# Optimization experiments

Hardware: AMD Instinct MI355X
Metric: run time of the kernel (lower is better)

Reference implementation:

```python
import jax, jax.numpy as jnp
import numpy as np

NA, NB, C = 50000, 50000, 128
E = 800000
S, IN, H, NBASES = 8, 64, 64, 8
NUM_LAYERS = 2
EPS = 1e-5


def setup_inputs() -> dict:
    key = jax.random.key(0)
    ks = jax.random.split(key, 16)
    inp = {
        'x_a': jax.random.normal(ks[0], (NA, C), jnp.float32),
        'x_b': jax.random.normal(ks[1], (NB, C), jnp.float32),
        'schema_x': jax.random.normal(ks[2], (S, IN), jnp.float32),
        'edge_ab': jax.random.randint(ks[3], (2, E), 0, NA, jnp.int32),
        'edge_ba': jax.random.randint(ks[4], (2, E), 0, NA, jnp.int32),
        'edge_aa': jax.random.randint(ks[5], (2, E), 0, NA, jnp.int32),
        'schema_edge_index': jax.random.randint(ks[6], (2, 24), 0, S, jnp.int32),
        'pre_W': jax.random.normal(ks[7], (H, IN), jnp.float32) * (1.0 / np.sqrt(IN)),
        'pre_b': jnp.zeros((H,), jnp.float32),
        'gcn_W': jax.random.normal(ks[8], (H, H), jnp.float32) * (1.0 / np.sqrt(H)),
        'gcn_b': jnp.zeros((H,), jnp.float32),
        'coeff_W': jax.random.normal(ks[9], (NBASES, 2 * H), jnp.float32) * (1.0 / np.sqrt(2 * H)),
        'coeff_b': jnp.zeros((NBASES,), jnp.float32),
        'bases': jax.random.normal(ks[10], (NUM_LAYERS, NBASES, C, C), jnp.float32) * (1.0 / np.sqrt(C)),
        'sage_bias': jnp.zeros((NUM_LAYERS, 3, C), jnp.float32),
        'ln_w': jnp.ones((NUM_LAYERS, 2, C), jnp.float32),
        'ln_b': jnp.zeros((NUM_LAYERS, 2, C), jnp.float32),
    }
    return inp


def _gcn_conv(x, ei, W, b):
    # PyG GCNConv: add self-loops, symmetric normalization, then linear.
    n = x.shape[0]
    loop = jnp.arange(n, dtype=ei.dtype)
    src = jnp.concatenate([ei[0], loop])
    dst = jnp.concatenate([ei[1], loop])
    deg = jax.ops.segment_sum(jnp.ones_like(dst, jnp.float32), dst, num_segments=n)
    dinv = jax.lax.rsqrt(jnp.maximum(deg, 1e-12))
    norm = dinv[src] * dinv[dst]  # [E+n]
    xw = x @ W.T  # [n, H]
    out = jax.ops.segment_sum(xw[src] * norm[:, None], dst, num_segments=n)
    return out + b


def _sage_conv(x_src, x_dst, ei, W, b):
    # PyG SAGEConv, aggr='mean': lin_l(mean_j x_src[j]) + lin_r(x_dst); lin_l.weight == lin_r.weight == W.
    n_dst = x_dst.shape[0]
    msg_sum = jax.ops.segment_sum(x_src[ei[0]], ei[1], num_segments=n_dst)
    cnt = jax.ops.segment_sum(jnp.ones(ei.shape[1], x_src.dtype), ei[1], num_segments=n_dst)
    mean = msg_sum / jnp.maximum(cnt, 1.0)[:, None]
    return (mean + x_dst) @ W.T + b


def _layer_norm(x, w, b):
    mu = jnp.mean(x, axis=-1, keepdims=True)
    var = jnp.mean(jnp.square(x - mu), axis=-1, keepdims=True)
    return (x - mu) * jax.lax.rsqrt(var + EPS) * w + b


def _edge_weight(sf_src, sf_dst, coeff_W, coeff_b, bases_l):
    combined = jnp.concatenate([sf_src, sf_dst], axis=0)  # [2H]
    coeffs = combined @ coeff_W.T + coeff_b  # [NBASES]
    return jnp.einsum('i,ijk->jk', coeffs, bases_l)  # [C, C]


def reference(x_a, x_b, schema_x, edge_ab, edge_ba, edge_aa, schema_edge_index,
              pre_W, pre_b, gcn_W, gcn_b, coeff_W, coeff_b, bases,
              sage_bias, ln_w, ln_b):
    # Schema GCN over the tiny table-level graph. table_to_index: a->0, b->1.
    h = schema_x @ pre_W.T + pre_b
    ori = h
    sf = jax.nn.relu(_gcn_conv(h, schema_edge_index, gcn_W, gcn_b))  # [S, H]

    for l in range(NUM_LAYERS):
        bases_l = bases[l]
        W_ab = _edge_weight(sf[0], sf[1], coeff_W, coeff_b, bases_l)
        W_ba = _edge_weight(sf[1], sf[0], coeff_W, coeff_b, bases_l)
        W_aa = _edge_weight(sf[0], sf[0], coeff_W, coeff_b, bases_l)
        # HeteroConv(aggr='sum'): sum SAGE outputs per destination node type.
        out_b = _sage_conv(x_a, x_b, edge_ab, W_ab, sage_bias[l, 0])
        out_a = (_sage_conv(x_b, x_a, edge_ba, W_ba, sage_bias[l, 1])
                 + _sage_conv(x_a, x_a, edge_aa, W_aa, sage_bias[l, 2]))
        x_a = jax.nn.relu(_layer_norm(out_a, ln_w[l, 0], ln_b[l, 0]))
        x_b = jax.nn.relu(_layer_norm(out_b, ln_w[l, 1], ln_b[l, 1]))

    return x_a, x_b, sf, ori
```

## Files before the change

### kernel.cpp

```cpp
#include <hip/hip_runtime.h>

#define NA 50000
#define NB 50000
#define NN 50000
#define CDIM 128
#define EDGES 800000
#define SS 8
#define INDIM 64
#define HDIM 64
#define NBASES 8
#define NBUCK 98
#define BSH 9

typedef __attribute__((ext_vector_type(8))) short bf16x8;
typedef __attribute__((ext_vector_type(4))) float f32x4;


__device__ __forceinline__ unsigned short f2bf(float f) {
    unsigned u = __float_as_uint(f);
    return (unsigned short)((u + 0x7FFFu + ((u >> 16) & 1u)) >> 16);
}

__global__ __launch_bounds__(512) void schema_kernel(
    const float* __restrict__ schema_x, const int* __restrict__ sei,
    const float* __restrict__ preW, const float* __restrict__ preb,
    const float* __restrict__ gcnW, const float* __restrict__ gcnb,
    const float* __restrict__ coW, const float* __restrict__ cob,
    float* __restrict__ out_sf, float* __restrict__ out_ori,
    float* __restrict__ coeffs)
{
    __shared__ float h[SS][HDIM];
    __shared__ float xw[SS][HDIM];
    __shared__ float sf[SS][HDIM];
    __shared__ float deg[SS];
    __shared__ float nrm[32];
    __shared__ int es[32], ed[32];

    int t = threadIdx.x;
    int i = t >> 6, j = t & 63;

    float acc = preb[j];
    for (int k = 0; k < INDIM; k++) acc += schema_x[i * INDIM + k] * preW[j * INDIM + k];
    h[i][j] = acc;
    out_ori[i * HDIM + j] = acc;
    if (t < SS) deg[t] = 0.0f;
    __syncthreads();

    if (t < 32) {
        int s, d;
        if (t < 24) { s = sei[t]; d = sei[24 + t]; }
        else        { s = t - 24; d = t - 24; }
        es[t] = s; ed[t] = d;
        atomicAdd(&deg[d], 1.0f);
    }
    __syncthreads();
    if (t < 32) {
        nrm[t] = rsqrtf(fmaxf(deg[es[t]], 1e-12f)) * rsqrtf(fmaxf(deg[ed[t]], 1e-12f));
    }
    float a2 = 0.0f;
    for (int k = 0; k < HDIM; k++) a2 += h[i][k] * gcnW[j * HDIM + k];
    xw[i][j] = a2;
    __syncthreads();

    float o = gcnb[j];
    for (int e = 0; e < 32; e++) {
        if (ed[e] == i) o += xw[es[e]][j] * nrm[e];
    }
    float s = fmaxf(o, 0.0f);
    sf[i][j] = s;
    out_sf[i * HDIM + j] = s;
    __syncthreads();

    if (t < 24) {
        int ty = t >> 3, ii = t & 7;
        int srow = (ty == 1) ? 1 : 0;
        int drow = (ty == 0) ? 1 : 0;
        float a = cob[ii];
        for (int k = 0; k < HDIM; k++) a += sf[srow][k] * coW[ii * (2 * HDIM) + k];
        for (int k = 0; k < HDIM; k++) a += sf[drow][k] * coW[ii * (2 * HDIM) + HDIM + k];
        coeffs[ty * 8 + ii] = a;
    }
}

__global__ __launch_bounds__(256) void build_w_kernel(
    const float* __restrict__ bases, const float* __restrict__ coeffs,
    unsigned short* __restrict__ Wbf)
{
    int idx = blockIdx.x * blockDim.x + threadIdx.x;
    int lt = idx >> 14;
    int jk = idx & 16383;
    int l = lt / 3, ty = lt % 3;
    float acc = 0.0f;
#pragma unroll
    for (int i = 0; i < NBASES; i++)
        acc += coeffs[ty * 8 + i] * bases[((size_t)(l * NBASES + i) << 14) + jk];
    Wbf[idx] = f2bf(acc);
}

__global__ __launch_bounds__(256) void tobf16_kernel(
    const float* __restrict__ in, unsigned short* __restrict__ out, int n)
{
    int i = (blockIdx.x * 256 + threadIdx.x) * 4;
    if (i >= n) return;
    float4 f = *(const float4*)(in + i);
    ushort4 o;
    o.x = f2bf(f.x); o.y = f2bf(f.y); o.z = f2bf(f.z); o.w = f2bf(f.w);
    *(ushort4*)(out + i) = o;
}

__global__ __launch_bounds__(256) void zero_rows_kernel(
    unsigned short* a0, unsigned short* b0, unsigned short* a1, unsigned short* b1)
{
    int t = threadIdx.x;
    int tab = t >> 6, w = t & 63;
    unsigned short* p = (tab == 0) ? a0 : (tab == 1) ? b0 : (tab == 2) ? a1 : b1;
    ((unsigned*)(p + (size_t)NN * CDIM))[w] = 0u;
}


__global__ __launch_bounds__(256) void bucket_count_kernel(
    const int* __restrict__ ab, const int* __restrict__ ba,
    const int* __restrict__ aa, int* __restrict__ bcnt)
{
    __shared__ int h[NBUCK];
    int t = threadIdx.x;
    int ty = blockIdx.y;
    const int* ei = (ty == 0) ? ab : (ty == 1) ? ba : aa;
    if (t < NBUCK) h[t] = 0;
    __syncthreads();
    int cb = blockIdx.x * 4096;
    int en = min(cb + 4096, EDGES);
    for (int e = cb + t; e < en; e += 256)
        atomicAdd(&h[ei[EDGES + e] >> BSH], 1);
    __syncthreads();
    if (t < NBUCK) atomicAdd(&bcnt[ty * NBUCK + t], h[t]);
}

__global__ __launch_bounds__(32) void bucket_scan_kernel(
    const int* __restrict__ bcnt, int* __restrict__ boff, int* __restrict__ bcur)
{
    int t = threadIdx.x;
    if (t < 3) {
        int run = 0;
        for (int i = 0; i < NBUCK; i++) {
            int c = bcnt[t * NBUCK + i];
            boff[t * (NBUCK + 1) + i] = run;
            bcur[t * NBUCK + i] = run;
            run += c;
        }
        boff[t * (NBUCK + 1) + NBUCK] = run;
    }
}

__global__ __launch_bounds__(256) void bucket_partition_kernel(
    const int* __restrict__ ab, const int* __restrict__ ba,
    const int* __restrict__ aa, int* __restrict__ bcur,
    unsigned* __restrict__ buf)
{
    __shared__ int h[NBUCK];
    __shared__ int basearr[NBUCK];
    __shared__ int cur[NBUCK];
    int t = threadIdx.x;
    int ty = blockIdx.y;
    const int* ei = (ty == 0) ? ab : (ty == 1) ? ba : aa;
    if (t < NBUCK) h[t] = 0;
    __syncthreads();
    int cb = blockIdx.x * 4096;
    int en = min(cb + 4096, EDGES);
    for (int e = cb + t; e < en; e += 256)
        atomicAdd(&h[ei[EDGES + e] >> BSH], 1);
    __syncthreads();
    if (t < NBUCK) {
        basearr[t] = atomicAdd(&bcur[ty * NBUCK + t], h[t]);
        cur[t] = 0;
    }
    __syncthreads();
    for (int e = cb + t; e < en; e += 256) {
        int src = ei[e], dst = ei[EDGES + e];
        int b = dst >> BSH;
        int r = atomicAdd(&cur[b], 1);
        buf[(size_t)ty * EDGES + basearr[b] + r] =
            ((unsigned)(dst & 511) << 16) | (unsigned)src;
    }
}

__global__ __launch_bounds__(256) void bucket_scatter_kernel(
    const unsigned* __restrict__ buf, const int* __restrict__ boff,
    int* __restrict__ rowptr, int* __restrict__ col)
{
    __shared__ int cnt[512];
    __shared__ int part[256];
    int t = threadIdx.x;
    int b = blockIdx.x, ty = blockIdx.y;
    int nstart = boff[ty * (NBUCK + 1) + b];
    int nend   = boff[ty * (NBUCK + 1) + b + 1];
    int n = nend - nstart;
    cnt[t] = 0; cnt[t + 256] = 0;
    __syncthreads();
    const unsigned* bb = buf + (size_t)ty * EDGES + nstart;
    for (int i = t; i < n; i += 256)
        atomicAdd(&cnt[bb[i] >> 16], 1);
    __syncthreads();
    int a0 = cnt[2 * t], a1 = cnt[2 * t + 1];
    int s = a0 + a1;
    part[t] = s;
    __syncthreads();
    for (int off = 1; off < 256; off <<= 1) {
        int v = (t >= off) ? part[t - off] : 0;
        __syncthreads();
        part[t] += v;
        __syncthreads();
    }
    int excl = part[t] - s;
    int p0 = excl, p1 = excl + a0;
    cnt[2 * t] = p0; cnt[2 * t + 1] = p1;
    int row0 = (b << BSH) + 2 * t;
    int rbase = ty * (NN + 1);
    if (row0 < NN)     rowptr[rbase + row0] = nstart + p0;
    if (row0 + 1 < NN) rowptr[rbase + row0 + 1] = nstart + p1;
    if (b == NBUCK - 1 && t == 255) rowptr[rbase + NN] = EDGES;
    __syncthreads();
    int* cc = col + (size_t)ty * EDGES + nstart;
    for (int i = t; i < n; i += 256) {
        unsigned pk = bb[i];
        int r = atomicAdd(&cnt[pk >> 16], 1);
        cc[r] = (int)(pk & 0xFFFFu);
    }
}


__device__ __forceinline__ float4 gather2_bf(
    const unsigned short* __restrict__ xsrc, const int* __restrict__ col,
    int s, int e, int half, int off)
{
    float4 g = {0.f, 0.f, 0.f, 0.f};
    int n = e - s;
    if (n > 0) {
        if (n <= 16) {
            int cs[8];
#pragma unroll
            for (int j = 0; j < 8; j++) {
                int slot = s + 2 * j + half;
                int cc = col[min(slot, e - 1)];
                cs[j] = (slot < e) ? cc : NN;
            }
            uint2 v[8];
#pragma unroll
            for (int j = 0; j < 8; j++)
                v[j] = *(const uint2*)(xsrc + (size_t)cs[j] * CDIM + off);
#pragma unroll
            for (int j = 0; j < 8; j++) {
                g.x += __uint_as_float(v[j].x << 16);
                g.y += __uint_as_float(v[j].x & 0xffff0000u);
                g.z += __uint_as_float(v[j].y << 16);
                g.w += __uint_as_float(v[j].y & 0xffff0000u);
            }
        } else {
            int cs[16];
#pragma unroll
            for (int j = 0; j < 16; j++) {
                int slot = s + 2 * j + half;
                int cc = col[min(slot, e - 1)];
                cs[j] = (slot < e) ? cc : NN;
            }
            uint2 v[16];
#pragma unroll
            for (int j = 0; j < 16; j++)
                v[j] = *(const uint2*)(xsrc + (size_t)cs[j] * CDIM + off);
#pragma unroll
            for (int j = 0; j < 16; j++) {
                g.x += __uint_as_float(v[j].x << 16);
                g.y += __uint_as_float(v[j].x & 0xffff0000u);
                g.z += __uint_as_float(v[j].y << 16);
                g.w += __uint_as_float(v[j].y & 0xffff0000u);
            }
            for (int b2 = s + 32; b2 < e; b2 += 16) {
#pragma unroll
                for (int j = 0; j < 8; j++) {
                    int slot = b2 + 2 * j + half;
                    int cc = col[min(slot, e - 1)];
                    int id = (slot < e) ? cc : NN;
                    uint2 vv = *(const uint2*)(xsrc + (size_t)id * CDIM + off);
                    g.x += __uint_as_float(vv.x << 16);
                    g.y += __uint_as_float(vv.x & 0xffff0000u);
                    g.z += __uint_as_float(vv.y << 16);
                    g.w += __uint_as_float(vv.y & 0xffff0000u);
                }
            }
        }
    }
    g.x += __shfl_xor(g.x, 32, 64);
    g.y += __shfl_xor(g.y, 32, 64);
    g.z += __shfl_xor(g.z, 32, 64);
    g.w += __shfl_xor(g.w, 32, 64);
    return g;
}

#define RROWS 32
#define USTR 136
#define SSTR 129

__global__ __launch_bounds__(256, 8) void fuse_b_kernel(
    const unsigned short* __restrict__ xsrc, const float* __restrict__ xdst,
    const int* __restrict__ rowptr, const int* __restrict__ col,
    const unsigned short* __restrict__ Wbf, const float* __restrict__ bias,
    const float* __restrict__ lnw, const float* __restrict__ lnb,
    float* __restrict__ xnext, unsigned short* __restrict__ xnext_bf)
{
    __shared__ float4 smraw[1032];
    unsigned short* Ubf = (unsigned short*)smraw;
    float* stage = (float*)smraw;
    int t = threadIdx.x;
    int base = blockIdx.x * RROWS;
    int wv = t >> 6;
    int lane = t & 63;
    int half = lane >> 5, cl = lane & 31;
    int off = cl << 2;

    for (int rr = 0; rr < RROWS / 4; rr++) {
        int r = rr * 4 + wv;
        int row = base + r;
        if (row < NN) {
            int s = rowptr[row], e = rowptr[row + 1];
            float4 g = gather2_bf(xsrc, col, s, e, half, off);
            if (half == 0) {
                float inv = 1.0f / (float)max(e - s, 1);
                const float4 xv = *(const float4*)(xdst + (size_t)row * CDIM + off);
                ushort4 o;
                o.x = f2bf(g.x * inv + xv.x);
                o.y = f2bf(g.y * inv + xv.y);
                o.z = f2bf(g.z * inv + xv.z);
                o.w = f2bf(g.w * inv + xv.w);
                *(ushort4*)&Ubf[r * USTR + off] = o;
            }
        } else if (half == 0) {
            *(ushort4*)&Ubf[r * USTR + off] = make_ushort4(0, 0, 0, 0);
        }
    }
    __syncthreads();

    int qd = lane >> 4;
    int ln16 = lane & 15;
    f32x4 acc00 = {0.f,0.f,0.f,0.f}, acc01 = acc00, acc10 = acc00, acc11 = acc00;
#pragma unroll
    for (int ks = 0; ks < 4; ks++) {
        int koff = ks * 32 + qd * 8;
        bf16x8 a0 = *(const bf16x8*)&Ubf[(ln16) * USTR + koff];
        bf16x8 a1 = *(const bf16x8*)&Ubf[(16 + ln16) * USTR + koff];
        bf16x8 b0 = *(const bf16x8*)&Wbf[(size_t)((2 * wv + 0) * 16 + ln16) * CDIM + koff];
        bf16x8 b1 = *(const bf16x8*)&Wbf[(size_t)((2 * wv + 1) * 16 + ln16) * CDIM + koff];
        acc00 = __builtin_amdgcn_mfma_f32_16x16x32_bf16(a0, b0, acc00, 0, 0, 0);
        acc01 = __builtin_amdgcn_mfma_f32_16x16x32_bf16(a0, b1, acc01, 0, 0, 0);
        acc10 = __builtin_amdgcn_mfma_f32_16x16x32_bf16(a1, b0, acc10, 0, 0, 0);
        acc11 = __builtin_amdgcn_mfma_f32_16x16x32_bf16(a1, b1, acc11, 0, 0, 0);
    }
    __syncthreads();
    {
        int c0 = (2 * wv + 0) * 16 + ln16;
        int c1 = (2 * wv + 1) * 16 + ln16;
#pragma unroll
        for (int i = 0; i < 4; i++) {
            int r0 = qd * 4 + i;
            stage[r0 * SSTR + c0] = acc00[i];
            stage[r0 * SSTR + c1] = acc01[i];
            stage[(16 + r0) * SSTR + c0] = acc10[i];
            stage[(16 + r0) * SSTR + c1] = acc11[i];
        }
    }
    __syncthreads();

    float b0v = bias[lane], b1v = bias[lane + 64];
    float lw0 = lnw[lane], lw1 = lnw[lane + 64];
    float lb0 = lnb[lane], lb1 = lnb[lane + 64];
    for (int rr = 0; rr < RROWS / 4; rr++) {
        int r = rr * 4 + wv;
        int row = base + r;
        if (row >= NN) continue;
        float v0 = stage[r * SSTR + lane] + b0v;
        float v1 = stage[r * SSTR + lane + 64] + b1v;
        float s = v0 + v1, s2 = v0 * v0 + v1 * v1;
#pragma unroll
        for (int o2 = 32; o2 > 0; o2 >>= 1) {
            s  += __shfl_xor(s,  o2, 64);
            s2 += __shfl_xor(s2, o2, 64);
        }
        float mu = s * (1.0f / CDIM);
        float var = s2 * (1.0f / CDIM) - mu * mu;
        float rs = rsqrtf(var + 1e-5f);
        float o0 = fmaxf((v0 - mu) * rs * lw0 + lb0, 0.0f);
        float o1 = fmaxf((v1 - mu) * rs * lw1 + lb1, 0.0f);
        size_t oi = (size_t)row * CDIM;
        xnext[oi + lane] = o0;
        xnext[oi + lane + 64] = o1;
        if (xnext_bf) {
            xnext_bf[oi + lane] = f2bf(o0);
            xnext_bf[oi + lane + 64] = f2bf(o1);
        }
    }
}

__global__ __launch_bounds__(256, 8) void fuse_a_kernel(
    const unsigned short* __restrict__ xsrc1, const int* __restrict__ rowptr1, const int* __restrict__ col1,
    const unsigned short* __restrict__ xsrc2, const int* __restrict__ rowptr2, const int* __restrict__ col2,
    const float* __restrict__ xdst,
    const unsigned short* __restrict__ W1bf, const unsigned short* __restrict__ W2bf,
    const float* __restrict__ bias1, const float* __restrict__ bias2,
    const float* __restrict__ lnw, const float* __restrict__ lnb,
    float* __restrict__ xnext, unsigned short* __restrict__ xnext_bf)
{
    __shared__ float4 smraw[1088];
    unsigned short* Ubf = (unsigned short*)smraw;
    unsigned short* Vbf = Ubf + RROWS * USTR;
    float* stage = (float*)smraw;
    int t = threadIdx.x;
    int base = blockIdx.x * RROWS;
    int wv = t >> 6;
    int lane = t & 63;
    int half = lane >> 5, cl = lane & 31;
    int off = cl << 2;

    for (int rr = 0; rr < RROWS / 4; rr++) {
        int r = rr * 4 + wv;
        int row = base + r;
        if (row < NN) {
            int s1 = rowptr1[row], e1 = rowptr1[row + 1];
            float4 g1 = gather2_bf(xsrc1, col1, s1, e1, half, off);
            int s2 = rowptr2[row], e2 = rowptr2[row + 1];
            float4 g2 = gather2_bf(xsrc2, col2, s2, e2, half, off);
            if (half == 0) {
                const float4 xv = *(const float4*)(xdst + (size_t)row * CDIM + off);
                float i1 = 1.0f / (float)max(e1 - s1, 1);
                float i2 = 1.0f / (float)max(e2 - s2, 1);
                ushort4 ou, ov;
                ou.x = f2bf(g1.x * i1 + xv.x); ou.y = f2bf(g1.y * i1 + xv.y);
                ou.z = f2bf(g1.z * i1 + xv.z); ou.w = f2bf(g1.w * i1 + xv.w);
                ov.x = f2bf(g2.x * i2 + xv.x); ov.y = f2bf(g2.y * i2 + xv.y);
                ov.z = f2bf(g2.z * i2 + xv.z); ov.w = f2bf(g2.w * i2 + xv.w);
                *(ushort4*)&Ubf[r * USTR + off] = ou;
                *(ushort4*)&Vbf[r * USTR + off] = ov;
            }
        } else if (half == 0) {
            *(ushort4*)&Ubf[r * USTR + off] = make_ushort4(0, 0, 0, 0);
            *(ushort4*)&Vbf[r * USTR + off] = make_ushort4(0, 0, 0, 0);
        }
    }
    __syncthreads();

    int qd = lane >> 4;
    int ln16 = lane & 15;
    f32x4 acc00 = {0.f,0.f,0.f,0.f}, acc01 = acc00, acc10 = acc00, acc11 = acc00;
#pragma unroll
    for (int ks = 0; ks < 4; ks++) {
        int koff = ks * 32 + qd * 8;
        bf16x8 aU0 = *(const bf16x8*)&Ubf[(ln16) * USTR + koff];
        bf16x8 aU1 = *(const bf16x8*)&Ubf[(16 + ln16) * USTR + koff];
        bf16x8 aV0 = *(const bf16x8*)&Vbf[(ln16) * USTR + koff];
        bf16x8 aV1 = *(const bf16x8*)&Vbf[(16 + ln16) * USTR + koff];
        size_t wrow0 = (size_t)((2 * wv + 0) * 16 + ln16) * CDIM + koff;
        size_t wrow1 = (size_t)((2 * wv + 1) * 16 + ln16) * CDIM + koff;
        bf16x8 b10 = *(const bf16x8*)&W1bf[wrow0];
        bf16x8 b11 = *(const bf16x8*)&W1bf[wrow1];
        bf16x8 b20 = *(const bf16x8*)&W2bf[wrow0];
        bf16x8 b21 = *(const bf16x8*)&W2bf[wrow1];
        acc00 = __builtin_amdgcn_mfma_f32_16x16x32_bf16(aU0, b10, acc00, 0, 0, 0);
        acc01 = __builtin_amdgcn_mfma_f32_16x16x32_bf16(aU0, b11, acc01, 0, 0, 0);
        acc10 = __builtin_amdgcn_mfma_f32_16x16x32_bf16(aU1, b10, acc10, 0, 0, 0);
        acc11 = __builtin_amdgcn_mfma_f32_16x16x32_bf16(aU1, b11, acc11, 0, 0, 0);
        acc00 = __builtin_amdgcn_mfma_f32_16x16x32_bf16(aV0, b20, acc00, 0, 0, 0);
        acc01 = __builtin_amdgcn_mfma_f32_16x16x32_bf16(aV0, b21, acc01, 0, 0, 0);
        acc10 = __builtin_amdgcn_mfma_f32_16x16x32_bf16(aV1, b20, acc10, 0, 0, 0);
        acc11 = __builtin_amdgcn_mfma_f32_16x16x32_bf16(aV1, b21, acc11, 0, 0, 0);
    }
    __syncthreads();
    {
        int c0 = (2 * wv + 0) * 16 + ln16;
        int c1 = (2 * wv + 1) * 16 + ln16;
#pragma unroll
        for (int i = 0; i < 4; i++) {
            int r0 = qd * 4 + i;
            stage[r0 * SSTR + c0] = acc00[i];
            stage[r0 * SSTR + c1] = acc01[i];
            stage[(16 + r0) * SSTR + c0] = acc10[i];
            stage[(16 + r0) * SSTR + c1] = acc11[i];
        }
    }
    __syncthreads();

    float b0v = bias1[lane] + bias2[lane];
    float b1v = bias1[lane + 64] + bias2[lane + 64];
    float lw0 = lnw[lane], lw1 = lnw[lane + 64];
    float lb0 = lnb[lane], lb1 = lnb[lane + 64];
    for (int rr = 0; rr < RROWS / 4; rr++) {
        int r = rr * 4 + wv;
        int row = base + r;
        if (row >= NN) continue;
        float v0 = stage[r * SSTR + lane] + b0v;
        float v1 = stage[r * SSTR + lane + 64] + b1v;
        float s = v0 + v1, s2 = v0 * v0 + v1 * v1;
#pragma unroll
        for (int o2 = 32; o2 > 0; o2 >>= 1) {
            s  += __shfl_xor(s,  o2, 64);
            s2 += __shfl_xor(s2, o2, 64);
        }
        float mu = s * (1.0f / CDIM);
        float var = s2 * (1.0f / CDIM) - mu * mu;
        float rs = rsqrtf(var + 1e-5f);
        float o0 = fmaxf((v0 - mu) * rs * lw0 + lb0, 0.0f);
        float o1 = fmaxf((v1 - mu) * rs * lw1 + lb1, 0.0f);
        size_t oi = (size_t)row * CDIM;
        xnext[oi + lane] = o0;
        xnext[oi + lane + 64] = o1;
        if (xnext_bf) {
            xnext_bf[oi + lane] = f2bf(o0);
            xnext_bf[oi + lane + 64] = f2bf(o1);
        }
    }
}

extern "C" void kernel_launch(void* const* d_in, const int* in_sizes, int n_in,
                              void* d_out, int out_size, void* d_ws, size_t ws_size,
                              hipStream_t stream)
{
    const float* x_a      = (const float*)d_in[0];
    const float* x_b      = (const float*)d_in[1];
    const float* schema_x = (const float*)d_in[2];
    const int*   e_ab     = (const int*)d_in[3];
    const int*   e_ba     = (const int*)d_in[4];
    const int*   e_aa     = (const int*)d_in[5];
    const int*   sei      = (const int*)d_in[6];
    const float* preW     = (const float*)d_in[7];
    const float* preb     = (const float*)d_in[8];
    const float* gcnW     = (const float*)d_in[9];
    const float* gcnb     = (const float*)d_in[10];
    const float* coW      = (const float*)d_in[11];
    const float* cob      = (const float*)d_in[12];
    const float* bases    = (const float*)d_in[13];
    const float* sbias    = (const float*)d_in[14];
    const float* lnw      = (const float*)d_in[15];
    const float* lnb      = (const float*)d_in[16];

    float* out     = (float*)d_out;
    float* out_xa  = out;
    float* out_xb  = out + 6400000;
    float* out_sf  = out + 12800000;
    float* out_ori = out + 12800512;

    float* ws = (float*)d_ws;
    int*      col    = (int*)ws;
    int*      rowptr = (int*)(ws + 2400000);
    unsigned* buf    = (unsigned*)(ws + 2550016);
    int*      bcnt   = (int*)(ws + 4950016);
    int*      boff   = (int*)(ws + 4950320);
    int*      bcur   = (int*)(ws + 4950624);
    float* xa_buf = ws + 4950928;
    float* xb_buf = ws + 11350928;
    unsigned short* Wbf = (unsigned short*)(ws + 17750928);
    float* coeffs = ws + 17800080;
    unsigned short* xa_bf0 = (unsigned short*)(ws + 17800112);
    unsigned short* xb_bf0 = (unsigned short*)(ws + 21000176);
    unsigned short* xa_bf1 = (unsigned short*)(ws + 24200240);
    unsigned short* xb_bf1 = (unsigned short*)(ws + 27400304);

    schema_kernel<<<1, 512, 0, stream>>>(schema_x, sei, preW, preb, gcnW, gcnb,
                                         coW, cob, out_sf, out_ori, coeffs);
    build_w_kernel<<<384, 256, 0, stream>>>(bases, coeffs, Wbf);

    tobf16_kernel<<<(NA * CDIM / 4 + 255) / 256, 256, 0, stream>>>(x_a, xa_bf0, NA * CDIM);
    tobf16_kernel<<<(NB * CDIM / 4 + 255) / 256, 256, 0, stream>>>(x_b, xb_bf0, NB * CDIM);
    zero_rows_kernel<<<1, 256, 0, stream>>>(xa_bf0, xb_bf0, xa_bf1, xb_bf1);

    hipMemsetAsync(bcnt, 0, 3 * NBUCK * sizeof(int), stream);
    dim3 cgrid((EDGES + 4095) / 4096, 3);
    bucket_count_kernel<<<cgrid, 256, 0, stream>>>(e_ab, e_ba, e_aa, bcnt);
    bucket_scan_kernel<<<1, 32, 0, stream>>>(bcnt, boff, bcur);
    bucket_partition_kernel<<<cgrid, 256, 0, stream>>>(e_ab, e_ba, e_aa, bcur, buf);
    dim3 sgrid(NBUCK, 3);
    bucket_scatter_kernel<<<sgrid, 256, 0, stream>>>(buf, boff, rowptr, col);

    const int* rp_ab = rowptr;
    const int* rp_ba = rowptr + (NN + 1);
    const int* rp_aa = rowptr + 2 * (NN + 1);
    const int* col_ab = col;
    const int* col_ba = col + EDGES;
    const int* col_aa = col + 2 * EDGES;

    const int fgrid = (NN + RROWS - 1) / RROWS;

    for (int l = 0; l < 2; l++) {
        const float* xa_cur = (l == 0) ? x_a : xa_buf;
        const float* xb_cur = (l == 0) ? x_b : xb_buf;
        const unsigned short* xa_bf = (l == 0) ? xa_bf0 : xa_bf1;
        const unsigned short* xb_bf = (l == 0) ? xb_bf0 : xb_bf1;
        const unsigned short* Wab = Wbf + (size_t)(l * 3 + 0) * 16384;
        const unsigned short* Wba = Wbf + (size_t)(l * 3 + 1) * 16384;
        const unsigned short* Waa = Wbf + (size_t)(l * 3 + 2) * 16384;
        float* xa_nxt = (l == 0) ? xa_buf : out_xa;
        float* xb_nxt = (l == 0) ? xb_buf : out_xb;
        unsigned short* xa_nbf = (l == 0) ? xa_bf1 : nullptr;
        unsigned short* xb_nbf = (l == 0) ? xb_bf1 : nullptr;

        fuse_b_kernel<<<fgrid, 256, 0, stream>>>(
            xa_bf, xb_cur, rp_ab, col_ab, Wab,
            sbias + (size_t)(l * 3 + 0) * 128,
            lnw + (size_t)(l * 2 + 1) * 128, lnb + (size_t)(l * 2 + 1) * 128,
            xb_nxt, xb_nbf);
        fuse_a_kernel<<<fgrid, 256, 0, stream>>>(
            xb_bf, rp_ba, col_ba, xa_bf, rp_aa, col_aa, xa_cur,
            Wba, Waa,
            sbias + (size_t)(l * 3 + 1) * 128, sbias + (size_t)(l * 3 + 2) * 128,
            lnw + (size_t)(l * 2 + 0) * 128, lnb + (size_t)(l * 2 + 0) * 128,
            xa_nxt, xa_nbf);
    }
}
```

Measured before the change: 549.4 us.

## Sub-sort CSR edges by source chunk and sweep chunks across block rows

The CSR build now sorts each destination row's edges by source-id chunk (13 chunks of 4096 rows) and keeps a per-(row, chunk) rowptr. The gather phase loops over chunks in the outer loop and the block's 8 rows per wave in the inner loop, so all waves read from the same source window at roughly the same time, aiming for better L2 locality on random gathers. The cost is a 13x larger rowptr array, more rowptr loads, short two-element gather loops with less memory-level parallelism, a bigger shared histogram in the scatter kernel, and lower occupancy from a reduced launch bound.

```diff
diff --git a/kernel.cpp b/kernel.cpp
--- a/kernel.cpp
+++ b/kernel.cpp
@@ -11,6 +11,14 @@
 #define NBASES 8
 #define NBUCK 98
 #define BSH 9
+#define NCHUNK 13
+#define CSH 12
+#define NKEY (512 * NCHUNK)
+#define RPSTR (NN * NCHUNK + 1)
+
+#define RROWS 32
+#define USTR 136
+#define SSTR 129
 
 typedef __attribute__((ext_vector_type(8))) short bf16x8;
 typedef __attribute__((ext_vector_type(4))) float f32x4;
@@ -188,119 +196,132 @@
     const unsigned* __restrict__ buf, const int* __restrict__ boff,
     int* __restrict__ rowptr, int* __restrict__ col)
 {
-    __shared__ int cnt[512];
+    __shared__ int cnt[NKEY];
     __shared__ int part[256];
     int t = threadIdx.x;
     int b = blockIdx.x, ty = blockIdx.y;
     int nstart = boff[ty * (NBUCK + 1) + b];
     int nend   = boff[ty * (NBUCK + 1) + b + 1];
     int n = nend - nstart;
-    cnt[t] = 0; cnt[t + 256] = 0;
+    for (int k = t; k < NKEY; k += 256) cnt[k] = 0;
     __syncthreads();
     const unsigned* bb = buf + (size_t)ty * EDGES + nstart;
-    for (int i = t; i < n; i += 256)
-        atomicAdd(&cnt[bb[i] >> 16], 1);
-    __syncthreads();
-    int a0 = cnt[2 * t], a1 = cnt[2 * t + 1];
-    int s = a0 + a1;
-    part[t] = s;
-    __syncthreads();
-    for (int off = 1; off < 256; off <<= 1) {
-        int v = (t >= off) ? part[t - off] : 0;
+    for (int i = t; i < n; i += 256) {
+        unsigned pk = bb[i];
+        int key = (int)(pk >> 16) * NCHUNK + (int)((pk & 0xFFFFu) >> CSH);
+        atomicAdd(&cnt[key], 1);
+    }
+    __syncthreads();
+    const int KPT = NKEY / 256;
+    int k0 = t * KPT;
+    int lc[KPT];
+    int lsum = 0;
+#pragma unroll
+    for (int j = 0; j < KPT; j++) { lc[j] = cnt[k0 + j]; lsum += lc[j]; }
+    part[t] = lsum;
+    __syncthreads();
+    for (int off2 = 1; off2 < 256; off2 <<= 1) {
+        int v = (t >= off2) ? part[t - off2] : 0;
         __syncthreads();
         part[t] += v;
         __syncthreads();
     }
-    int excl = part[t] - s;
-    int p0 = excl, p1 = excl + a0;
-    cnt[2 * t] = p0; cnt[2 * t + 1] = p1;
-    int row0 = (b << BSH) + 2 * t;
-    int rbase = ty * (NN + 1);
-    if (row0 < NN)     rowptr[rbase + row0] = nstart + p0;
-    if (row0 + 1 < NN) rowptr[rbase + row0 + 1] = nstart + p1;
-    if (b == NBUCK - 1 && t == 255) rowptr[rbase + NN] = EDGES;
+    int run = part[t] - lsum;
+    {
+        int row_in_b = k0 / NCHUNK;
+        int ch = k0 - row_in_b * NCHUNK;
+        int rowg = (b << BSH) + row_in_b;
+        size_t rpbase = (size_t)ty * RPSTR;
+#pragma unroll
+        for (int j = 0; j < KPT; j++) {
+            cnt[k0 + j] = run;
+            if (rowg < NN)
+                rowptr[rpbase + (size_t)rowg * NCHUNK + ch] = nstart + run;
+            run += lc[j];
+            ch++;
+            if (ch == NCHUNK) { ch = 0; rowg++; }
+        }
+        if (b == NBUCK - 1 && t == 255)
+            rowptr[rpbase + (size_t)NN * NCHUNK] = EDGES;
+    }
     __syncthreads();
     int* cc = col + (size_t)ty * EDGES + nstart;
     for (int i = t; i < n; i += 256) {
         unsigned pk = bb[i];
-        int r = atomicAdd(&cnt[pk >> 16], 1);
+        int key = (int)(pk >> 16) * NCHUNK + (int)((pk & 0xFFFFu) >> CSH);
+        int r = atomicAdd(&cnt[key], 1);
         cc[r] = (int)(pk & 0xFFFFu);
     }
 }
 
 
-__device__ __forceinline__ float4 gather2_bf(
+__device__ __forceinline__ void gseg_acc(
     const unsigned short* __restrict__ xsrc, const int* __restrict__ col,
-    int s, int e, int half, int off)
-{
-    float4 g = {0.f, 0.f, 0.f, 0.f};
-    int n = e - s;
-    if (n > 0) {
-        if (n <= 16) {
-            int cs[8];
-#pragma unroll
-            for (int j = 0; j < 8; j++) {
-                int slot = s + 2 * j + half;
-                int cc = col[min(slot, e - 1)];
-                cs[j] = (slot < e) ? cc : NN;
+    int s, int e, int half, int off, float4* g)
+{
+    for (int b0 = s; b0 < e; b0 += 4) {
+        int sl0 = b0 + half;
+        int sl1 = b0 + 2 + half;
+        int c0 = col[min(sl0, e - 1)];
+        int c1 = col[min(sl1, e - 1)];
+        int i0 = (sl0 < e) ? c0 : NN;
+        int i1 = (sl1 < e) ? c1 : NN;
+        uint2 v0 = *(const uint2*)(xsrc + (size_t)i0 * CDIM + off);
+        uint2 v1 = *(const uint2*)(xsrc + (size_t)i1 * CDIM + off);
+        g->x += __uint_as_float(v0.x << 16) + __uint_as_float(v1.x << 16);
+        g->y += __uint_as_float(v0.x & 0xffff0000u) + __uint_as_float(v1.x & 0xffff0000u);
+        g->z += __uint_as_float(v0.y << 16) + __uint_as_float(v1.y << 16);
+        g->w += __uint_as_float(v0.y & 0xffff0000u) + __uint_as_float(v1.y & 0xffff0000u);
+    }
+}
+
+__device__ __forceinline__ void sweep_store(
+    const unsigned short* __restrict__ xsrc, const int* __restrict__ rowptr,
+    const int* __restrict__ col, const float* __restrict__ xdst,
+    unsigned short* __restrict__ Obf,
+    int base, int wv, int half, int off)
+{
+    float4 g[8];
+#pragma unroll
+    for (int rr = 0; rr < 8; rr++) g[rr] = make_float4(0.f, 0.f, 0.f, 0.f);
+    for (int c = 0; c < NCHUNK; c++) {
+#pragma unroll
+        for (int rr = 0; rr < 8; rr++) {
+            int row = base + rr * 4 + wv;
+            if (row < NN) {
+                int idx = row * NCHUNK + c;
+                int s = rowptr[idx], e = rowptr[idx + 1];
+                if (s < e) gseg_acc(xsrc, col, s, e, half, off, &g[rr]);
             }
-            uint2 v[8];
-#pragma unroll
-            for (int j = 0; j < 8; j++)
-                v[j] = *(const uint2*)(xsrc + (size_t)cs[j] * CDIM + off);
-#pragma unroll
-            for (int j = 0; j < 8; j++) {
-                g.x += __uint_as_float(v[j].x << 16);
-                g.y += __uint_as_float(v[j].x & 0xffff0000u);
-                g.z += __uint_as_float(v[j].y << 16);
-                g.w += __uint_as_float(v[j].y & 0xffff0000u);
+        }
+    }
+#pragma unroll
+    for (int rr = 0; rr < 8; rr++) {
+        int r = rr * 4 + wv;
+        int row = base + r;
+        float4 gg = g[rr];
+        gg.x += __shfl_xor(gg.x, 32, 64);
+        gg.y += __shfl_xor(gg.y, 32, 64);
+        gg.z += __shfl_xor(gg.z, 32, 64);
+        gg.w += __shfl_xor(gg.w, 32, 64);
+        if (half == 0) {
+            ushort4 o = make_ushort4(0, 0, 0, 0);
+            if (row < NN) {
+                int s0 = rowptr[row * NCHUNK];
+                int e0 = rowptr[row * NCHUNK + NCHUNK];
+                float inv = 1.0f / (float)max(e0 - s0, 1);
+                const float4 xv = *(const float4*)(xdst + (size_t)row * CDIM + off);
+                o.x = f2bf(gg.x * inv + xv.x);
+                o.y = f2bf(gg.y * inv + xv.y);
+                o.z = f2bf(gg.z * inv + xv.z);
+                o.w = f2bf(gg.w * inv + xv.w);
             }
-        } else {
-            int cs[16];
-#pragma unroll
-            for (int j = 0; j < 16; j++) {
-                int slot = s + 2 * j + half;
-                int cc = col[min(slot, e - 1)];
-                cs[j] = (slot < e) ? cc : NN;
-            }
-            uint2 v[16];
-#pragma unroll
-            for (int j = 0; j < 16; j++)
-                v[j] = *(const uint2*)(xsrc + (size_t)cs[j] * CDIM + off);
-#pragma unroll
-            for (int j = 0; j < 16; j++) {
-                g.x += __uint_as_float(v[j].x << 16);
-                g.y += __uint_as_float(v[j].x & 0xffff0000u);
-                g.z += __uint_as_float(v[j].y << 16);
-                g.w += __uint_as_float(v[j].y & 0xffff0000u);
-            }
-            for (int b2 = s + 32; b2 < e; b2 += 16) {
-#pragma unroll
-                for (int j = 0; j < 8; j++) {
-                    int slot = b2 + 2 * j + half;
-                    int cc = col[min(slot, e - 1)];
-                    int id = (slot < e) ? cc : NN;
-                    uint2 vv = *(const uint2*)(xsrc + (size_t)id * CDIM + off);
-                    g.x += __uint_as_float(vv.x << 16);
-                    g.y += __uint_as_float(vv.x & 0xffff0000u);
-                    g.z += __uint_as_float(vv.y << 16);
-                    g.w += __uint_as_float(vv.y & 0xffff0000u);
-                }
-            }
-        }
-    }
-    g.x += __shfl_xor(g.x, 32, 64);
-    g.y += __shfl_xor(g.y, 32, 64);
-    g.z += __shfl_xor(g.z, 32, 64);
-    g.w += __shfl_xor(g.w, 32, 64);
-    return g;
-}
-
-#define RROWS 32
-#define USTR 136
-#define SSTR 129
-
-__global__ __launch_bounds__(256, 8) void fuse_b_kernel(
+            *(ushort4*)&Obf[r * USTR + off] = o;
+        }
+    }
+}
+
+__global__ __launch_bounds__(256, 6) void fuse_b_kernel(
     const unsigned short* __restrict__ xsrc, const float* __restrict__ xdst,
     const int* __restrict__ rowptr, const int* __restrict__ col,
     const unsigned short* __restrict__ Wbf, const float* __restrict__ bias,
@@ -317,26 +338,7 @@
     int half = lane >> 5, cl = lane & 31;
     int off = cl << 2;
 
-    for (int rr = 0; rr < RROWS / 4; rr++) {
-        int r = rr * 4 + wv;
-        int row = base + r;
-        if (row < NN) {
-            int s = rowptr[row], e = rowptr[row + 1];
-            float4 g = gather2_bf(xsrc, col, s, e, half, off);
-            if (half == 0) {
-                float inv = 1.0f / (float)max(e - s, 1);
-                const float4 xv = *(const float4*)(xdst + (size_t)row * CDIM + off);
-                ushort4 o;
-                o.x = f2bf(g.x * inv + xv.x);
-                o.y = f2bf(g.y * inv + xv.y);
-                o.z = f2bf(g.z * inv + xv.z);
-                o.w = f2bf(g.w * inv + xv.w);
-                *(ushort4*)&Ubf[r * USTR + off] = o;
-            }
-        } else if (half == 0) {
-            *(ushort4*)&Ubf[r * USTR + off] = make_ushort4(0, 0, 0, 0);
-        }
-    }
+    sweep_store(xsrc, rowptr, col, xdst, Ubf, base, wv, half, off);
     __syncthreads();
 
     int qd = lane >> 4;
@@ -399,7 +401,7 @@
     }
 }
 
-__global__ __launch_bounds__(256, 8) void fuse_a_kernel(
+__global__ __launch_bounds__(256, 6) void fuse_a_kernel(
     const unsigned short* __restrict__ xsrc1, const int* __restrict__ rowptr1, const int* __restrict__ col1,
     const unsigned short* __restrict__ xsrc2, const int* __restrict__ rowptr2, const int* __restrict__ col2,
     const float* __restrict__ xdst,
@@ -419,31 +421,8 @@
     int half = lane >> 5, cl = lane & 31;
     int off = cl << 2;
 
-    for (int rr = 0; rr < RROWS / 4; rr++) {
-        int r = rr * 4 + wv;
-        int row = base + r;
-        if (row < NN) {
-            int s1 = rowptr1[row], e1 = rowptr1[row + 1];
-            float4 g1 = gather2_bf(xsrc1, col1, s1, e1, half, off);
-            int s2 = rowptr2[row], e2 = rowptr2[row + 1];
-            float4 g2 = gather2_bf(xsrc2, col2, s2, e2, half, off);
-            if (half == 0) {
-                const float4 xv = *(const float4*)(xdst + (size_t)row * CDIM + off);
-                float i1 = 1.0f / (float)max(e1 - s1, 1);
-                float i2 = 1.0f / (float)max(e2 - s2, 1);
-                ushort4 ou, ov;
-                ou.x = f2bf(g1.x * i1 + xv.x); ou.y = f2bf(g1.y * i1 + xv.y);
-                ou.z = f2bf(g1.z * i1 + xv.z); ou.w = f2bf(g1.w * i1 + xv.w);
-                ov.x = f2bf(g2.x * i2 + xv.x); ov.y = f2bf(g2.y * i2 + xv.y);
-                ov.z = f2bf(g2.z * i2 + xv.z); ov.w = f2bf(g2.w * i2 + xv.w);
-                *(ushort4*)&Ubf[r * USTR + off] = ou;
-                *(ushort4*)&Vbf[r * USTR + off] = ov;
-            }
-        } else if (half == 0) {
-            *(ushort4*)&Ubf[r * USTR + off] = make_ushort4(0, 0, 0, 0);
-            *(ushort4*)&Vbf[r * USTR + off] = make_ushort4(0, 0, 0, 0);
-        }
-    }
+    sweep_store(xsrc1, rowptr1, col1, xdst, Ubf, base, wv, half, off);
+    sweep_store(xsrc2, rowptr2, col2, xdst, Vbf, base, wv, half, off);
     __syncthreads();
 
     int qd = lane >> 4;
@@ -548,18 +527,18 @@
     float* ws = (float*)d_ws;
     int*      col    = (int*)ws;
     int*      rowptr = (int*)(ws + 2400000);
-    unsigned* buf    = (unsigned*)(ws + 2550016);
-    int*      bcnt   = (int*)(ws + 4950016);
-    int*      boff   = (int*)(ws + 4950320);
-    int*      bcur   = (int*)(ws + 4950624);
-    float* xa_buf = ws + 4950928;
-    float* xb_buf = ws + 11350928;
-    unsigned short* Wbf = (unsigned short*)(ws + 17750928);
-    float* coeffs = ws + 17800080;
-    unsigned short* xa_bf0 = (unsigned short*)(ws + 17800112);
-    unsigned short* xb_bf0 = (unsigned short*)(ws + 21000176);
-    unsigned short* xa_bf1 = (unsigned short*)(ws + 24200240);
-    unsigned short* xb_bf1 = (unsigned short*)(ws + 27400304);
+    unsigned* buf    = (unsigned*)(ws + 4350016);
+    int*      bcnt   = (int*)(ws + 6750016);
+    int*      boff   = (int*)(ws + 6750320);
+    int*      bcur   = (int*)(ws + 6750624);
+    float* xa_buf = ws + 6750928;
+    float* xb_buf = ws + 13150928;
+    unsigned short* Wbf = (unsigned short*)(ws + 19550928);
+    float* coeffs = ws + 19600080;
+    unsigned short* xa_bf0 = (unsigned short*)(ws + 19600112);
+    unsigned short* xb_bf0 = (unsigned short*)(ws + 22800176);
+    unsigned short* xa_bf1 = (unsigned short*)(ws + 26000240);
+    unsigned short* xb_bf1 = (unsigned short*)(ws + 29200304);
 
     schema_kernel<<<1, 512, 0, stream>>>(schema_x, sei, preW, preb, gcnW, gcnb,
                                          coW, cob, out_sf, out_ori, coeffs);
@@ -578,8 +557,8 @@
     bucket_scatter_kernel<<<sgrid, 256, 0, stream>>>(buf, boff, rowptr, col);
 
     const int* rp_ab = rowptr;
-    const int* rp_ba = rowptr + (NN + 1);
-    const int* rp_aa = rowptr + 2 * (NN + 1);
+    const int* rp_ba = rowptr + RPSTR;
+    const int* rp_aa = rowptr + 2 * RPSTR;
     const int* col_ab = col;
     const int* col_ba = col + EDGES;
     const int* col_aa = col + 2 * EDGES;
```

After: 1.208 ms. +119.8%, slower.

## Interleave gathers of two rows per wave to raise memory-level parallelism

Applied to the files above, without the earlier changes.

The per-row gather helper is replaced by inline code that issues the column-index loads and feature loads for two independent neighbour lists (two rows in fuse_b, two edge types in fuse_a) before accumulating. The first 32 slots are always loaded unconditionally instead of branching on degree, and out-of-range slots are padded to a zero row. This puts more outstanding memory requests in flight per wave. In exchange, register pressure rises, so launch bounds drop from 8 to 4 waves per SIMD, which lowers occupancy.

```diff
diff --git a/kernel.cpp b/kernel.cpp
--- a/kernel.cpp
+++ b/kernel.cpp
@@ -12,6 +12,10 @@
 #define NBUCK 98
 #define BSH 9
 
+#define RROWS 32
+#define USTR 136
+#define SSTR 129
+
 typedef __attribute__((ext_vector_type(8))) short bf16x8;
 typedef __attribute__((ext_vector_type(4))) float f32x4;
 
@@ -229,78 +233,13 @@
 }
 
 
-__device__ __forceinline__ float4 gather2_bf(
-    const unsigned short* __restrict__ xsrc, const int* __restrict__ col,
-    int s, int e, int half, int off)
-{
-    float4 g = {0.f, 0.f, 0.f, 0.f};
-    int n = e - s;
-    if (n > 0) {
-        if (n <= 16) {
-            int cs[8];
-#pragma unroll
-            for (int j = 0; j < 8; j++) {
-                int slot = s + 2 * j + half;
-                int cc = col[min(slot, e - 1)];
-                cs[j] = (slot < e) ? cc : NN;
-            }
-            uint2 v[8];
-#pragma unroll
-            for (int j = 0; j < 8; j++)
-                v[j] = *(const uint2*)(xsrc + (size_t)cs[j] * CDIM + off);
-#pragma unroll
-            for (int j = 0; j < 8; j++) {
-                g.x += __uint_as_float(v[j].x << 16);
-                g.y += __uint_as_float(v[j].x & 0xffff0000u);
-                g.z += __uint_as_float(v[j].y << 16);
-                g.w += __uint_as_float(v[j].y & 0xffff0000u);
-            }
-        } else {
-            int cs[16];
-#pragma unroll
-            for (int j = 0; j < 16; j++) {
-                int slot = s + 2 * j + half;
-                int cc = col[min(slot, e - 1)];
-                cs[j] = (slot < e) ? cc : NN;
-            }
-            uint2 v[16];
-#pragma unroll
-            for (int j = 0; j < 16; j++)
-                v[j] = *(const uint2*)(xsrc + (size_t)cs[j] * CDIM + off);
-#pragma unroll
-            for (int j = 0; j < 16; j++) {
-                g.x += __uint_as_float(v[j].x << 16);
-                g.y += __uint_as_float(v[j].x & 0xffff0000u);
-                g.z += __uint_as_float(v[j].y << 16);
-                g.w += __uint_as_float(v[j].y & 0xffff0000u);
-            }
-            for (int b2 = s + 32; b2 < e; b2 += 16) {
-#pragma unroll
-                for (int j = 0; j < 8; j++) {
-                    int slot = b2 + 2 * j + half;
-                    int cc = col[min(slot, e - 1)];
-                    int id = (slot < e) ? cc : NN;
-                    uint2 vv = *(const uint2*)(xsrc + (size_t)id * CDIM + off);
-                    g.x += __uint_as_float(vv.x << 16);
-                    g.y += __uint_as_float(vv.x & 0xffff0000u);
-                    g.z += __uint_as_float(vv.y << 16);
-                    g.w += __uint_as_float(vv.y & 0xffff0000u);
-                }
-            }
-        }
-    }
-    g.x += __shfl_xor(g.x, 32, 64);
-    g.y += __shfl_xor(g.y, 32, 64);
-    g.z += __shfl_xor(g.z, 32, 64);
-    g.w += __shfl_xor(g.w, 32, 64);
-    return g;
-}
-
-#define RROWS 32
-#define USTR 136
-#define SSTR 129
-
-__global__ __launch_bounds__(256, 8) void fuse_b_kernel(
+#define ACC4(gv, vv)                                            \
+    gv.x += __uint_as_float((vv).x << 16);                      \
+    gv.y += __uint_as_float((vv).x & 0xffff0000u);              \
+    gv.z += __uint_as_float((vv).y << 16);                      \
+    gv.w += __uint_as_float((vv).y & 0xffff0000u);
+
+__global__ __launch_bounds__(256, 4) void fuse_b_kernel(
     const unsigned short* __restrict__ xsrc, const float* __restrict__ xdst,
     const int* __restrict__ rowptr, const int* __restrict__ col,
     const unsigned short* __restrict__ Wbf, const float* __restrict__ bias,
@@ -317,24 +256,87 @@
     int half = lane >> 5, cl = lane & 31;
     int off = cl << 2;
 
-    for (int rr = 0; rr < RROWS / 4; rr++) {
-        int r = rr * 4 + wv;
-        int row = base + r;
-        if (row < NN) {
-            int s = rowptr[row], e = rowptr[row + 1];
-            float4 g = gather2_bf(xsrc, col, s, e, half, off);
-            if (half == 0) {
-                float inv = 1.0f / (float)max(e - s, 1);
-                const float4 xv = *(const float4*)(xdst + (size_t)row * CDIM + off);
-                ushort4 o;
-                o.x = f2bf(g.x * inv + xv.x);
-                o.y = f2bf(g.y * inv + xv.y);
-                o.z = f2bf(g.z * inv + xv.z);
-                o.w = f2bf(g.w * inv + xv.w);
-                *(ushort4*)&Ubf[r * USTR + off] = o;
+    for (int k = 0; k < 4; k++) {
+        int rA = (2 * k) * 4 + wv;
+        int rB = rA + 4;
+        int rowA = base + rA, rowB = base + rB;
+        int sA = 0, eA = 0, sB = 0, eB = 0;
+        if (rowA < NN) { sA = rowptr[rowA]; eA = rowptr[rowA + 1]; }
+        if (rowB < NN) { sB = rowptr[rowB]; eB = rowptr[rowB + 1]; }
+        int csA[16], csB[16];
+#pragma unroll
+        for (int j = 0; j < 16; j++) {
+            int sl = sA + 2 * j + half;
+            int cc = col[min(sl, EDGES - 1)];
+            csA[j] = (sl < eA) ? cc : NN;
+        }
+#pragma unroll
+        for (int j = 0; j < 16; j++) {
+            int sl = sB + 2 * j + half;
+            int cc = col[min(sl, EDGES - 1)];
+            csB[j] = (sl < eB) ? cc : NN;
+        }
+        uint2 vA[16], vB[16];
+#pragma unroll
+        for (int j = 0; j < 16; j++)
+            vA[j] = *(const uint2*)(xsrc + (size_t)csA[j] * CDIM + off);
+#pragma unroll
+        for (int j = 0; j < 16; j++)
+            vB[j] = *(const uint2*)(xsrc + (size_t)csB[j] * CDIM + off);
+        float4 gA = make_float4(0.f, 0.f, 0.f, 0.f);
+        float4 gB = make_float4(0.f, 0.f, 0.f, 0.f);
+#pragma unroll
+        for (int j = 0; j < 16; j++) { ACC4(gA, vA[j]) }
+#pragma unroll
+        for (int j = 0; j < 16; j++) { ACC4(gB, vB[j]) }
+        for (int b2 = sA + 32; b2 < eA; b2 += 16) {
+#pragma unroll
+            for (int j = 0; j < 8; j++) {
+                int sl = b2 + 2 * j + half;
+                int cc = col[min(sl, EDGES - 1)];
+                int id = (sl < eA) ? cc : NN;
+                uint2 vv = *(const uint2*)(xsrc + (size_t)id * CDIM + off);
+                ACC4(gA, vv)
             }
-        } else if (half == 0) {
-            *(ushort4*)&Ubf[r * USTR + off] = make_ushort4(0, 0, 0, 0);
+        }
+        for (int b2 = sB + 32; b2 < eB; b2 += 16) {
+#pragma unroll
+            for (int j = 0; j < 8; j++) {
+                int sl = b2 + 2 * j + half;
+                int cc = col[min(sl, EDGES - 1)];
+                int id = (sl < eB) ? cc : NN;
+                uint2 vv = *(const uint2*)(xsrc + (size_t)id * CDIM + off);
+                ACC4(gB, vv)
+            }
+        }
+        gA.x += __shfl_xor(gA.x, 32, 64);
+        gA.y += __shfl_xor(gA.y, 32, 64);
+        gA.z += __shfl_xor(gA.z, 32, 64);
+        gA.w += __shfl_xor(gA.w, 32, 64);
+        gB.x += __shfl_xor(gB.x, 32, 64);
+        gB.y += __shfl_xor(gB.y, 32, 64);
+        gB.z += __shfl_xor(gB.z, 32, 64);
+        gB.w += __shfl_xor(gB.w, 32, 64);
+        if (half == 0) {
+            ushort4 oA = make_ushort4(0, 0, 0, 0), oB = oA;
+            if (rowA < NN) {
+                float inv = 1.0f / (float)max(eA - sA, 1);
+                const float4 xv = *(const float4*)(xdst + (size_t)rowA * CDIM + off);
+                oA.x = f2bf(gA.x * inv + xv.x);
+                oA.y = f2bf(gA.y * inv + xv.y);
+                oA.z = f2bf(gA.z * inv + xv.z);
+                oA.w = f2bf(gA.w * inv + xv.w);
+            }
+            if (rowB < NN) {
+                float inv = 1.0f / (float)max(eB - sB, 1);
+                const float4 xv = *(const float4*)(xdst + (size_t)rowB * CDIM + off);
+                oB.x = f2bf(gB.x * inv + xv.x);
+                oB.y = f2bf(gB.y * inv + xv.y);
+                oB.z = f2bf(gB.z * inv + xv.z);
+                oB.w = f2bf(gB.w * inv + xv.w);
+            }
+            *(ushort4*)&Ubf[rA * USTR + off] = oA;
+            *(ushort4*)&Ubf[rB * USTR + off] = oB;
         }
     }
     __syncthreads();
@@ -399,7 +401,7 @@
     }
 }
 
-__global__ __launch_bounds__(256, 8) void fuse_a_kernel(
+__global__ __launch_bounds__(256, 4) void fuse_a_kernel(
     const unsigned short* __restrict__ xsrc1, const int* __restrict__ rowptr1, const int* __restrict__ col1,
     const unsigned short* __restrict__ xsrc2, const int* __restrict__ rowptr2, const int* __restrict__ col2,
     const float* __restrict__ xdst,
@@ -419,29 +421,81 @@
     int half = lane >> 5, cl = lane & 31;
     int off = cl << 2;
 
-    for (int rr = 0; rr < RROWS / 4; rr++) {
+    for (int rr = 0; rr < 8; rr++) {
         int r = rr * 4 + wv;
         int row = base + r;
+        int s1 = 0, e1 = 0, s2 = 0, e2 = 0;
         if (row < NN) {
-            int s1 = rowptr1[row], e1 = rowptr1[row + 1];
-            float4 g1 = gather2_bf(xsrc1, col1, s1, e1, half, off);
-            int s2 = rowptr2[row], e2 = rowptr2[row + 1];
-            float4 g2 = gather2_bf(xsrc2, col2, s2, e2, half, off);
-            if (half == 0) {
+            s1 = rowptr1[row]; e1 = rowptr1[row + 1];
+            s2 = rowptr2[row]; e2 = rowptr2[row + 1];
+        }
+        int cs1[16], cs2[16];
+#pragma unroll
+        for (int j = 0; j < 16; j++) {
+            int sl = s1 + 2 * j + half;
+            int cc = col1[min(sl, EDGES - 1)];
+            cs1[j] = (sl < e1) ? cc : NN;
+        }
+#pragma unroll
+        for (int j = 0; j < 16; j++) {
+            int sl = s2 + 2 * j + half;
+            int cc = col2[min(sl, EDGES - 1)];
+            cs2[j] = (sl < e2) ? cc : NN;
+        }
+        uint2 v1[16], v2[16];
+#pragma unroll
+        for (int j = 0; j < 16; j++)
+            v1[j] = *(const uint2*)(xsrc1 + (size_t)cs1[j] * CDIM + off);
+#pragma unroll
+        for (int j = 0; j < 16; j++)
+            v2[j] = *(const uint2*)(xsrc2 + (size_t)cs2[j] * CDIM + off);
+        float4 g1 = make_float4(0.f, 0.f, 0.f, 0.f);
+        float4 g2 = make_float4(0.f, 0.f, 0.f, 0.f);
+#pragma unroll
+        for (int j = 0; j < 16; j++) { ACC4(g1, v1[j]) }
+#pragma unroll
+        for (int j = 0; j < 16; j++) { ACC4(g2, v2[j]) }
+        for (int b2 = s1 + 32; b2 < e1; b2 += 16) {
+#pragma unroll
+            for (int j = 0; j < 8; j++) {
+                int sl = b2 + 2 * j + half;
+                int cc = col1[min(sl, EDGES - 1)];
+                int id = (sl < e1) ? cc : NN;
+                uint2 vv = *(const uint2*)(xsrc1 + (size_t)id * CDIM + off);
+                ACC4(g1, vv)
+            }
+        }
+        for (int b2 = s2 + 32; b2 < e2; b2 += 16) {
+#pragma unroll
+            for (int j = 0; j < 8; j++) {
+                int sl = b2 + 2 * j + half;
+                int cc = col2[min(sl, EDGES - 1)];
+                int id = (sl < e2) ? cc : NN;
+                uint2 vv = *(const uint2*)(xsrc2 + (size_t)id * CDIM + off);
+                ACC4(g2, vv)
+            }
+        }
+        g1.x += __shfl_xor(g1.x, 32, 64);
+        g1.y += __shfl_xor(g1.y, 32, 64);
+        g1.z += __shfl_xor(g1.z, 32, 64);
+        g1.w += __shfl_xor(g1.w, 32, 64);
+        g2.x += __shfl_xor(g2.x, 32, 64);
+        g2.y += __shfl_xor(g2.y, 32, 64);
+        g2.z += __shfl_xor(g2.z, 32, 64);
+        g2.w += __shfl_xor(g2.w, 32, 64);
+        if (half == 0) {
+            ushort4 ou = make_ushort4(0, 0, 0, 0), ov = ou;
+            if (row < NN) {
                 const float4 xv = *(const float4*)(xdst + (size_t)row * CDIM + off);
                 float i1 = 1.0f / (float)max(e1 - s1, 1);
                 float i2 = 1.0f / (float)max(e2 - s2, 1);
-                ushort4 ou, ov;
                 ou.x = f2bf(g1.x * i1 + xv.x); ou.y = f2bf(g1.y * i1 + xv.y);
                 ou.z = f2bf(g1.z * i1 + xv.z); ou.w = f2bf(g1.w * i1 + xv.w);
                 ov.x = f2bf(g2.x * i2 + xv.x); ov.y = f2bf(g2.y * i2 + xv.y);
                 ov.z = f2bf(g2.z * i2 + xv.z); ov.w = f2bf(g2.w * i2 + xv.w);
-                *(ushort4*)&Ubf[r * USTR + off] = ou;
-                *(ushort4*)&Vbf[r * USTR + off] = ov;
             }
-        } else if (half == 0) {
-            *(ushort4*)&Ubf[r * USTR + off] = make_ushort4(0, 0, 0, 0);
-            *(ushort4*)&Vbf[r * USTR + off] = make_ushort4(0, 0, 0, 0);
+            *(ushort4*)&Ubf[r * USTR + off] = ou;
+            *(ushort4*)&Vbf[r * USTR + off] = ov;
         }
     }
     __syncthreads();
```

Result: slower. 576.5 us (+4.9%).
